# Kernel tuning notes

Measured on AMD Instinct MI355X. Metric: run time of the kernel, lower is better.

## Reference

```python
import jax, jax.numpy as jnp
import numpy as np

EPS = 1e-5

def _gn(x, w, b):
    # GroupNorm with 1 group on [N, C]: normalize each row over C, then affine.
    mu = jnp.mean(x, axis=-1, keepdims=True)
    var = jnp.mean((x - mu) ** 2, axis=-1, keepdims=True)
    return (x - mu) * jax.lax.rsqrt(var + EPS) * w + b

def setup_inputs() -> dict:
    key = jax.random.key(0)
    ks = jax.random.split(key, 24)
    N_AGT, N_CTX, E, D, NC = 50000, 100000, 500000, 128, 2
    s = 0.05  # weight init scale
    inp = {
        "agts": jax.random.normal(ks[0], (N_AGT, D), jnp.float32),
        "ctx": jax.random.normal(ks[1], (N_CTX, D), jnp.float32),
        "agt_ctrs": jax.random.normal(ks[2], (N_AGT, NC), jnp.float32),
        "ctx_ctrs": jax.random.normal(ks[3], (N_CTX, NC), jnp.float32),
        "hi": jax.random.randint(ks[4], (E,), 0, N_AGT, jnp.int32),
        "wi": jax.random.randint(ks[5], (E,), 0, N_CTX, jnp.int32),
        # dist MLP: Linear(2->128, bias) + ReLU, then Linear(128->128 no bias)+GN+ReLU
        "Wd1": jax.random.normal(ks[6], (D, NC), jnp.float32) * s,
        "bd1": jnp.zeros((D,), jnp.float32),
        "Wd2": jax.random.normal(ks[7], (D, D), jnp.float32) * s,
        "gd2w": jnp.ones((D,), jnp.float32), "gd2b": jnp.zeros((D,), jnp.float32),
        # query: Linear(128->128 no bias)+GN+ReLU
        "Wq": jax.random.normal(ks[8], (D, D), jnp.float32) * s,
        "gqw": jnp.ones((D,), jnp.float32), "gqb": jnp.zeros((D,), jnp.float32),
        # ctx MLP: Linear(384->128 no bias)+GN+ReLU, then Linear(128->128 no bias)
        "Wc1": jax.random.normal(ks[9], (D, 3 * D), jnp.float32) * s,
        "gc1w": jnp.ones((D,), jnp.float32), "gc1b": jnp.zeros((D,), jnp.float32),
        "Wc2": jax.random.normal(ks[10], (D, D), jnp.float32) * s,
        # agt linear (no bias), post-scatter GN, final Linear(no bias)+GN
        "Wa": jax.random.normal(ks[11], (D, D), jnp.float32) * s,
        "gnw": jnp.ones((D,), jnp.float32), "gnb": jnp.zeros((D,), jnp.float32),
        "Wl": jax.random.normal(ks[12], (D, D), jnp.float32) * s,
        "glw": jnp.ones((D,), jnp.float32), "glb": jnp.zeros((D,), jnp.float32),
    }
    return inp

def reference(agts, ctx, agt_ctrs, ctx_ctrs, hi, wi,
              Wd1, bd1, Wd2, gd2w, gd2b, Wq, gqw, gqb,
              Wc1, gc1w, gc1b, Wc2, Wa, gnw, gnb, Wl, glw, glb):
    res = agts
    # dist branch: relative center offsets of edges -> MLP
    d = agt_ctrs[hi] - ctx_ctrs[wi]                    # [E, 2]
    d = jax.nn.relu(d @ Wd1.T + bd1)                   # [E, 128]
    d = jax.nn.relu(_gn(d @ Wd2.T, gd2w, gd2b))        # [E, 128]
    # query branch: gathered agent features
    q = jax.nn.relu(_gn(agts[hi] @ Wq.T, gqw, gqb))    # [E, 128]
    # ctx branch: concat(dist, query, gathered ctx) -> MLP
    c = jnp.concatenate([d, q, ctx[wi]], axis=1)       # [E, 384]
    c = jax.nn.relu(_gn(c @ Wc1.T, gc1w, gc1b))        # [E, 128]
    c = c @ Wc2.T                                      # [E, 128]
    # scatter-add messages back to agents
    a = agts @ Wa.T
    a = a.at[hi].add(c)
    a = jax.nn.relu(_gn(a, gnw, gnb))
    a = _gn(a @ Wl.T, glw, glb)
    return jax.nn.relu(a + res)
```

## Files before the change

### kernel.cpp

```cpp
#include <hip/hip_runtime.h>
#include <hip/hip_bf16.h>

#define D 128
#define TM 64
#define APITCH 136
#define WSLICE 16384

typedef __attribute__((ext_vector_type(8))) short short8;
typedef __attribute__((ext_vector_type(4))) float f32x4;
typedef __attribute__((ext_vector_type(2))) float f32x2;

__device__ __forceinline__ short f2bf(float f) {
    union { float f; unsigned u; } v; v.f = f;
    unsigned r = v.u + 0x7fffu + ((v.u >> 16) & 1u);
    return (short)(r >> 16);
}
__device__ __forceinline__ float bflo(unsigned v) {
    union { unsigned u; float f; } t; t.u = v << 16; return t.f;
}
__device__ __forceinline__ float bfhi(unsigned v) {
    union { unsigned u; float f; } t; t.u = v & 0xffff0000u; return t.f;
}
__device__ __forceinline__ unsigned pkbf(float a, float b) {
    return (unsigned)(unsigned short)f2bf(a) | ((unsigned)(unsigned short)f2bf(b) << 16);
}

struct TileLDS {
    short A[TM * APITCH];
    f32x2 red[TM][4][4];
    f32x2 mr[TM];
    int hi_s[TM];
    int wi_s[TM];
};

struct WPA { const float* src[8]; int pitch[8]; int coloff[8]; };

__global__ __launch_bounds__(256)
void k_wprep(WPA a, short* __restrict__ wf) {
    int slice = blockIdx.x & 7, chunk = blockIdx.x >> 3;
    int tid = threadIdx.x, lane = tid & 63;
    int slot = chunk * 4 + (tid >> 6);
    int w = slot >> 3, t = (slot >> 2) & 1, ks = slot & 3;
    int lr = lane & 15, kh = lane >> 4;
    const float* src = a.src[slice];
    int row = w * 32 + t * 16 + lr;
    int col0 = a.coloff[slice] + ks * 32 + kh * 8;
    short8 v;
#pragma unroll
    for (int j = 0; j < 8; ++j) v[j] = f2bf(src[(size_t)row * a.pitch[slice] + col0 + j]);
    *(short8*)&wf[(size_t)slice * WSLICE + ((size_t)slot * 64 + lane) * 8] = v;
}

__device__ __forceinline__ void load_wset_pre(const short* wf, int slice, int w, int lane,
                                              short8 frag[2][4]) {
    const short8* p = (const short8*)(wf + (size_t)slice * WSLICE);
#pragma unroll
    for (int t = 0; t < 2; ++t)
#pragma unroll
        for (int ks = 0; ks < 4; ++ks)
            frag[t][ks] = p[((w * 2 + t) * 4 + ks) * 64 + lane];
}

__device__ __forceinline__ void wave_gemm(const short* A, const short8 frag[2][4],
                                          int lr, int kh, f32x4 acc[4][2]) {
#pragma unroll
    for (int mt = 0; mt < 4; ++mt)
#pragma unroll
        for (int t = 0; t < 2; ++t)
            acc[mt][t] = (f32x4){0.f, 0.f, 0.f, 0.f};
#pragma unroll
    for (int ks = 0; ks < 4; ++ks) {
        short8 a[4];
#pragma unroll
        for (int mt = 0; mt < 4; ++mt)
            a[mt] = *(const short8*)&A[(mt * 16 + lr) * APITCH + ks * 32 + kh * 8];
#pragma unroll
        for (int mt = 0; mt < 4; ++mt)
#pragma unroll
            for (int t = 0; t < 2; ++t)
                acc[mt][t] = __builtin_amdgcn_mfma_f32_16x16x32_bf16(a[mt], frag[t][ks], acc[mt][t], 0, 0, 0);
    }
}

__device__ __forceinline__ void store_acc_global(float* Y, long rbase, int M,
                                                 const f32x4 acc[4][2], int lane, int w) {
    int lr = lane & 15, hh = lane >> 4;
#pragma unroll
    for (int mt = 0; mt < 4; ++mt)
#pragma unroll
        for (int t = 0; t < 2; ++t)
#pragma unroll
            for (int r = 0; r < 4; ++r) {
                int row = mt * 16 + hh * 4 + r;
                if (rbase + row < M)
                    Y[(size_t)(rbase + row) * D + w * 32 + t * 16 + lr] = acc[mt][t][r];
            }
}

__device__ __forceinline__ void store_acc_pk(unsigned* Y, long rbase, int M,
                                             const f32x4 acc[4][2], int lane, int w) {
    int lr = lane & 15, hh = lane >> 4;
#pragma unroll
    for (int mt = 0; mt < 4; ++mt)
#pragma unroll
        for (int r = 0; r < 4; ++r) {
            int row = mt * 16 + hh * 4 + r;
            if (rbase + row < M)
                Y[(size_t)(rbase + row) * 64 + w * 16 + lr] = pkbf(acc[mt][0][r], acc[mt][1][r]);
        }
}

__device__ __forceinline__ void gn_stats(TileLDS& L, const f32x4 acc[4][2],
                                         int tid, int lane, int w) {
    int lr = lane & 15, hh = lane >> 4;
#pragma unroll
    for (int mt = 0; mt < 4; ++mt)
#pragma unroll
        for (int r = 0; r < 4; ++r) {
            float s = acc[mt][0][r] + acc[mt][1][r];
            float q = acc[mt][0][r] * acc[mt][0][r] + acc[mt][1][r] * acc[mt][1][r];
            s += __shfl_xor(s, 1); q += __shfl_xor(q, 1);
            s += __shfl_xor(s, 2); q += __shfl_xor(q, 2);
            if ((lr & 3) == mt) {
                int row = mt * 16 + hh * 4 + r;
                L.red[row][w][lr >> 2] = (f32x2){s, q};
            }
        }
    __syncthreads();
    if (tid < TM) {
        float s = 0.f, q = 0.f;
        const f32x2* p = (const f32x2*)L.red[tid];
#pragma unroll
        for (int i = 0; i < 16; ++i) { f32x2 v = p[i]; s += v[0]; q += v[1]; }
        float mu = s * (1.f / 128.f);
        float var = q * (1.f / 128.f) - mu * mu;
        L.mr[tid] = (f32x2){mu, rsqrtf(var + 1e-5f)};
    }
    __syncthreads();
}

__device__ __forceinline__ void gn_reg(TileLDS& L, const f32x4 acc[4][2],
                                       float gw0, float gb0, float gw1, float gb1,
                                       int tid, int lane, int w) {
    gn_stats(L, acc, tid, lane, w);
    int lr = lane & 15, hh = lane >> 4, n0 = w * 32;
#pragma unroll
    for (int mt = 0; mt < 4; ++mt)
#pragma unroll
        for (int r = 0; r < 4; ++r) {
            int row = mt * 16 + hh * 4 + r;
            f32x2 m = L.mr[row];
            float v0 = (acc[mt][0][r] - m[0]) * m[1] * gw0 + gb0;
            float v1 = (acc[mt][1][r] - m[0]) * m[1] * gw1 + gb1;
            L.A[row * APITCH + n0 + lr]      = f2bf(fmaxf(v0, 0.f));
            L.A[row * APITCH + n0 + 16 + lr] = f2bf(fmaxf(v1, 0.f));
        }
    __syncthreads();
}

__device__ __forceinline__ void stage_rows_to_A(TileLDS& L, const float* X, long rbase, int M, int tid) {
#pragma unroll
    for (int it = 0; it < 8; ++it) {
        int chunk = tid + it * 256;
        int row = chunk >> 5, c4 = chunk & 31;
        long r = rbase + row;
        float4 v = (r < M) ? *(const float4*)&X[(size_t)r * D + c4 * 4] : make_float4(0.f, 0.f, 0.f, 0.f);
        short* a = &L.A[row * APITCH + c4 * 4];
        a[0] = f2bf(v.x); a[1] = f2bf(v.y); a[2] = f2bf(v.z); a[3] = f2bf(v.w);
    }
}

__global__ void k_hist(const int* __restrict__ hi, int* __restrict__ cnt, int E) {
    int i = blockIdx.x * 256 + threadIdx.x;
    if (i < E) atomicAdd(&cnt[hi[i]], 1);
}

__global__ void k_scan(const int* __restrict__ cnt, int* __restrict__ offs,
                       int* __restrict__ cursor, int n) {
    __shared__ int wsum[4];
    __shared__ int carry_s;
    int tid = threadIdx.x, lane = tid & 63, w = tid >> 6;
    if (tid == 0) carry_s = 0;
    __syncthreads();
    for (int base = 0; base < n; base += 256) {
        int i = base + tid;
        int v = (i < n) ? cnt[i] : 0;
        int x = v;
#pragma unroll
        for (int d = 1; d < 64; d <<= 1) {
            int t = __shfl_up(x, d);
            if (lane >= d) x += t;
        }
        if (lane == 63) wsum[w] = x;
        __syncthreads();
        int woff = 0;
        for (int j = 0; j < w; ++j) woff += wsum[j];
        int carry = carry_s;
        int excl = carry + woff + x - v;
        if (i < n) { offs[i] = excl; cursor[i] = excl; }
        __syncthreads();
        if (tid == 255) carry_s = carry + woff + x;
        __syncthreads();
    }
    if (tid == 0) offs[n] = carry_s;
}

__global__ void k_fill(const int* __restrict__ hi, int* __restrict__ cursor,
                       int* __restrict__ eidx, int E) {
    int i = blockIdx.x * 256 + threadIdx.x;
    if (i < E) {
        int p = atomicAdd(&cursor[hi[i]], 1);
        eidx[p] = i;
    }
}

__global__ __launch_bounds__(256, 3)
void k_qpath(const float* __restrict__ agts, const short* __restrict__ wf,
             const float* __restrict__ gqw, const float* __restrict__ gqb,
             unsigned* __restrict__ qp32, float* __restrict__ abuf, int M, int ntiles) {
    __shared__ TileLDS L;
    int tid = threadIdx.x;
    int lane = tid & 63, w = tid >> 6;
    int lr = lane & 15, kh = lane >> 4;
    int n0 = w * 32;
    short8 fa[2][4], fq[2][4], fcq[2][4];
    load_wset_pre(wf, 0, w, lane, fa);
    load_wset_pre(wf, 1, w, lane, fq);
    load_wset_pre(wf, 3, w, lane, fcq);
    float gw0 = gqw[n0 + lr], gw1 = gqw[n0 + 16 + lr];
    float gb0 = gqb[n0 + lr], gb1 = gqb[n0 + 16 + lr];

    for (int tile = blockIdx.x; tile < ntiles; tile += gridDim.x) {
        long rbase = (long)tile * TM;
        stage_rows_to_A(L, agts, rbase, M, tid);
        __syncthreads();
        f32x4 acc[4][2];
        wave_gemm(L.A, fa, lr, kh, acc);
        store_acc_global(abuf, rbase, M, acc, lane, w);
        wave_gemm(L.A, fq, lr, kh, acc);
        gn_reg(L, acc, gw0, gb0, gw1, gb1, tid, lane, w);
        wave_gemm(L.A, fcq, lr, kh, acc);
        store_acc_pk(qp32, rbase, M, acc, lane, w);
        __syncthreads();
    }
}

__global__ __launch_bounds__(256, 4)
void k_ctx(const float* __restrict__ ctx, const short* __restrict__ wf,
           unsigned* __restrict__ cp32, int M, int ntiles) {
    __shared__ TileLDS L;
    int tid = threadIdx.x;
    int lane = tid & 63, w = tid >> 6;
    int lr = lane & 15, kh = lane >> 4;
    short8 fc[2][4];
    load_wset_pre(wf, 4, w, lane, fc);
    for (int tile = blockIdx.x; tile < ntiles; tile += gridDim.x) {
        long rbase = (long)tile * TM;
        stage_rows_to_A(L, ctx, rbase, M, tid);
        __syncthreads();
        f32x4 acc[4][2];
        wave_gemm(L.A, fc, lr, kh, acc);
        store_acc_pk(cp32, rbase, M, acc, lane, w);
        __syncthreads();
    }
}

__global__ __launch_bounds__(256, 3)
void k_edge(const float* __restrict__ agt_ctrs, const float* __restrict__ ctx_ctrs,
            const int* __restrict__ hi, const int* __restrict__ wi,
            const float* __restrict__ Wd1, const float* __restrict__ bd1,
            const short* __restrict__ wf,
            const float* __restrict__ gd2w, const float* __restrict__ gd2b,
            const float* __restrict__ gc1w, const float* __restrict__ gc1b,
            const unsigned* __restrict__ qp32, const unsigned* __restrict__ cp32,
            short* __restrict__ ebuf, int E, int ntiles) {
    __shared__ TileLDS L;
    int tid = threadIdx.x;
    int lane = tid & 63, w = tid >> 6;
    int lr = lane & 15, kh = lane >> 4;
    int n0 = w * 32;
    short8 fd2[2][4], fc1[2][4], fc2[2][4];
    load_wset_pre(wf, 5, w, lane, fd2);
    load_wset_pre(wf, 2, w, lane, fc1);
    load_wset_pre(wf, 6, w, lane, fc2);
    float g2w0 = gd2w[n0 + lr], g2w1 = gd2w[n0 + 16 + lr];
    float g2b0 = gd2b[n0 + lr], g2b1 = gd2b[n0 + 16 + lr];
    float g1w0 = gc1w[n0 + lr], g1w1 = gc1w[n0 + 16 + lr];
    float g1b0 = gc1b[n0 + lr], g1b1 = gc1b[n0 + 16 + lr];

    for (int tile = blockIdx.x; tile < ntiles; tile += gridDim.x) {
        long ebase = (long)tile * TM;
        if (tid < TM) {
            long e = ebase + tid;
            L.hi_s[tid] = (e < E) ? hi[e] : 0;
            L.wi_s[tid] = (e < E) ? wi[e] : 0;
        }
        {
            int row = tid >> 2, q4 = tid & 3;
            long e = ebase + row;
            bool valid = e < E;
            float dd0 = 0.f, dd1 = 0.f;
            if (valid) {
                int h = hi[e], c = wi[e];
                dd0 = agt_ctrs[h * 2 + 0] - ctx_ctrs[c * 2 + 0];
                dd1 = agt_ctrs[h * 2 + 1] - ctx_ctrs[c * 2 + 1];
            }
#pragma unroll
            for (int cb = 0; cb < 4; ++cb) {
                short8 ov;
#pragma unroll
                for (int j = 0; j < 8; ++j) {
                    int c = q4 * 32 + cb * 8 + j;
                    float v = valid ? fmaxf(Wd1[c * 2 + 0] * dd0 + Wd1[c * 2 + 1] * dd1 + bd1[c], 0.f) : 0.f;
                    ov[j] = f2bf(v);
                }
                *(short8*)&L.A[row * APITCH + q4 * 32 + cb * 8] = ov;
            }
        }
        __syncthreads();
        f32x4 acc[4][2];
        wave_gemm(L.A, fd2, lr, kh, acc);
        gn_reg(L, acc, g2w0, g2b0, g2w1, g2b1, tid, lane, w);
        wave_gemm(L.A, fc1, lr, kh, acc);
#pragma unroll
        for (int mt = 0; mt < 4; ++mt)
#pragma unroll
            for (int r = 0; r < 4; ++r) {
                int row = mt * 16 + kh * 4 + r;
                unsigned vq = qp32[(size_t)L.hi_s[row] * 64 + w * 16 + lr];
                unsigned vc = cp32[(size_t)L.wi_s[row] * 64 + w * 16 + lr];
                acc[mt][0][r] += bflo(vq) + bflo(vc);
                acc[mt][1][r] += bfhi(vq) + bfhi(vc);
            }
        gn_reg(L, acc, g1w0, g1b0, g1w1, g1b1, tid, lane, w);
        wave_gemm(L.A, fc2, lr, kh, acc);
#pragma unroll
        for (int mt = 0; mt < 4; ++mt)
#pragma unroll
            for (int r = 0; r < 4; ++r) {
                int erow = mt * 16 + kh * 4 + r;
                long e = ebase + erow;
                if (e < E) {
                    short* dst = ebuf + (size_t)e * D;
                    dst[n0 + lr]      = f2bf(acc[mt][0][r]);
                    dst[n0 + 16 + lr] = f2bf(acc[mt][1][r]);
                }
            }
        __syncthreads();
    }
}

__global__ __launch_bounds__(256, 4)
void k_final(const float* __restrict__ abuf, const float* __restrict__ agts,
             const short* __restrict__ ebuf, const int* __restrict__ offs,
             const int* __restrict__ eidx, const short* __restrict__ wf,
             const float* __restrict__ gnw, const float* __restrict__ gnb,
             const float* __restrict__ glw, const float* __restrict__ glb,
             float* __restrict__ out, int M, int ntiles) {
    __shared__ TileLDS L;
    int tid = threadIdx.x;
    int lane = tid & 63, w = tid >> 6;
    int lr = lane & 15, kh = lane >> 4;
    int n0 = w * 32;
    short8 fl[2][4];
    load_wset_pre(wf, 7, w, lane, fl);
    float gw0 = glw[n0 + lr], gw1 = glw[n0 + 16 + lr];
    float gb0 = glb[n0 + lr], gb1 = glb[n0 + 16 + lr];

    for (int tile = blockIdx.x; tile < ntiles; tile += gridDim.x) {
        long rbase = (long)tile * TM;
        int row = tid >> 2, q4 = tid & 3;
        long r = rbase + row;
        float x[32];
        {
            const float4* src = (const float4*)(abuf + (size_t)r * D + q4 * 32);
#pragma unroll
            for (int i = 0; i < 8; ++i) {
                float4 v = (r < M) ? src[i] : make_float4(0.f, 0.f, 0.f, 0.f);
                x[i * 4 + 0] = v.x; x[i * 4 + 1] = v.y; x[i * 4 + 2] = v.z; x[i * 4 + 3] = v.w;
            }
            if (r < M) {
                int s0 = offs[r], e1 = offs[r + 1];
                for (int p = s0; p < e1; ++p) {
                    int e = eidx[p];
                    const unsigned* er = (const unsigned*)(ebuf + (size_t)e * D + q4 * 32);
#pragma unroll
                    for (int j = 0; j < 16; ++j) {
                        unsigned v = er[j];
                        x[j * 2 + 0] += bflo(v);
                        x[j * 2 + 1] += bfhi(v);
                    }
                }
            }
            float s = 0.f, q = 0.f;
#pragma unroll
            for (int i = 0; i < 32; ++i) { s += x[i]; q += x[i] * x[i]; }
            L.red[row][q4][0] = (f32x2){s, q};
        }
        __syncthreads();
        if (tid < TM) {
            float s = 0.f, q = 0.f;
#pragma unroll
            for (int i = 0; i < 4; ++i) { f32x2 v = L.red[tid][i][0]; s += v[0]; q += v[1]; }
            float mu = s * (1.f / 128.f);
            float var = q * (1.f / 128.f) - mu * mu;
            L.mr[tid] = (f32x2){mu, rsqrtf(var + 1e-5f)};
        }
        __syncthreads();
        {
            f32x2 m = L.mr[row];
#pragma unroll
            for (int cb = 0; cb < 4; ++cb) {
                short8 ov;
#pragma unroll
                for (int j = 0; j < 8; ++j) {
                    int c = q4 * 32 + cb * 8 + j;
                    float v = (x[cb * 8 + j] - m[0]) * m[1] * gnw[c] + gnb[c];
                    ov[j] = f2bf(fmaxf(v, 0.f));
                }
                *(short8*)&L.A[row * APITCH + q4 * 32 + cb * 8] = ov;
            }
        }
        __syncthreads();
        f32x4 acc[4][2];
        wave_gemm(L.A, fl, lr, kh, acc);
        gn_stats(L, acc, tid, lane, w);
#pragma unroll
        for (int mt = 0; mt < 4; ++mt)
#pragma unroll
            for (int rr = 0; rr < 4; ++rr) {
                int orow = mt * 16 + kh * 4 + rr;
                long gr = rbase + orow;
                if (gr < M) {
                    f32x2 m = L.mr[orow];
                    float v0 = (acc[mt][0][rr] - m[0]) * m[1] * gw0 + gb0;
                    float v1 = (acc[mt][1][rr] - m[0]) * m[1] * gw1 + gb1;
                    v0 += agts[(size_t)gr * D + n0 + lr];
                    v1 += agts[(size_t)gr * D + n0 + 16 + lr];
                    out[(size_t)gr * D + n0 + lr]      = fmaxf(v0, 0.f);
                    out[(size_t)gr * D + n0 + 16 + lr] = fmaxf(v1, 0.f);
                }
            }
        __syncthreads();
    }
}

extern "C" void kernel_launch(void* const* d_in, const int* in_sizes, int n_in,
                              void* d_out, int out_size, void* d_ws, size_t ws_size,
                              hipStream_t stream) {
    const float* agts     = (const float*)d_in[0];
    const float* ctx      = (const float*)d_in[1];
    const float* agt_ctrs = (const float*)d_in[2];
    const float* ctx_ctrs = (const float*)d_in[3];
    const int*   hi       = (const int*)d_in[4];
    const int*   wi       = (const int*)d_in[5];
    const float* Wd1 = (const float*)d_in[6];
    const float* bd1 = (const float*)d_in[7];
    const float* Wd2 = (const float*)d_in[8];
    const float* gd2w = (const float*)d_in[9];
    const float* gd2b = (const float*)d_in[10];
    const float* Wq  = (const float*)d_in[11];
    const float* gqw = (const float*)d_in[12];
    const float* gqb = (const float*)d_in[13];
    const float* Wc1 = (const float*)d_in[14];
    const float* gc1w = (const float*)d_in[15];
    const float* gc1b = (const float*)d_in[16];
    const float* Wc2 = (const float*)d_in[17];
    const float* Wa  = (const float*)d_in[18];
    const float* gnw = (const float*)d_in[19];
    const float* gnb = (const float*)d_in[20];
    const float* Wl  = (const float*)d_in[21];
    const float* glw = (const float*)d_in[22];
    const float* glb = (const float*)d_in[23];

    int N_AGT = in_sizes[0] / D;
    int N_CTX = in_sizes[1] / D;
    int E     = in_sizes[4];
    float* out = (float*)d_out;

    short*    wf   = (short*)d_ws;
    unsigned* qp32 = (unsigned*)(wf + 8 * WSLICE);
    unsigned* cp32 = qp32 + (size_t)N_AGT * 64;
    float*    abuf = (float*)(cp32 + (size_t)N_CTX * 64);
    short*    ebuf = (short*)(abuf + (size_t)N_AGT * D);
    int*      cnt    = (int*)(ebuf + (size_t)E * D);
    int*      offs   = cnt + N_AGT;
    int*      cursor = offs + N_AGT + 1;
    int*      eidx   = cursor + N_AGT;

    int tq = (N_AGT + TM - 1) / TM;
    int tc = (N_CTX + TM - 1) / TM;
    int te = (E + TM - 1) / TM;
    int ge = (E + 255) / 256;
    int gq = tq < 768 ? tq : 768;
    int gc = tc < 768 ? tc : 768;
    int gE = te < 1536 ? te : 1536;
    int gf = tq < 768 ? tq : 768;

    WPA wpa;
    wpa.src[0] = Wa;  wpa.pitch[0] = 128; wpa.coloff[0] = 0;
    wpa.src[1] = Wq;  wpa.pitch[1] = 128; wpa.coloff[1] = 0;
    wpa.src[2] = Wc1; wpa.pitch[2] = 384; wpa.coloff[2] = 0;
    wpa.src[3] = Wc1; wpa.pitch[3] = 384; wpa.coloff[3] = 128;
    wpa.src[4] = Wc1; wpa.pitch[4] = 384; wpa.coloff[4] = 256;
    wpa.src[5] = Wd2; wpa.pitch[5] = 128; wpa.coloff[5] = 0;
    wpa.src[6] = Wc2; wpa.pitch[6] = 128; wpa.coloff[6] = 0;
    wpa.src[7] = Wl;  wpa.pitch[7] = 128; wpa.coloff[7] = 0;

    hipMemsetAsync(cnt, 0, (size_t)N_AGT * sizeof(int), stream);
    k_wprep<<<64, 256, 0, stream>>>(wpa, wf);
    k_hist<<<ge, 256, 0, stream>>>(hi, cnt, E);
    k_scan<<<1, 256, 0, stream>>>(cnt, offs, cursor, N_AGT);
    k_fill<<<ge, 256, 0, stream>>>(hi, cursor, eidx, E);

    k_qpath<<<gq, 256, 0, stream>>>(agts, wf, gqw, gqb, qp32, abuf, N_AGT, tq);
    k_ctx<<<gc, 256, 0, stream>>>(ctx, wf, cp32, N_CTX, tc);
    k_edge<<<gE, 256, 0, stream>>>(agt_ctrs, ctx_ctrs, hi, wi, Wd1, bd1, wf,
                                   gd2w, gd2b, gc1w, gc1b, qp32, cp32, ebuf, E, te);
    k_final<<<gf, 256, 0, stream>>>(abuf, agts, ebuf, offs, eidx, wf,
                                    gnw, gnb, glw, glb, out, N_AGT, tq);
}
```

Baseline: 870.0 us.

## Process edges in agent-sorted order and write packed bf16 edge messages

The fill kernel now writes hi and wi permuted into agent-sorted order instead of an edge-index list. k_edge processes edges in that order, so k_final can read each agent's messages as one contiguous stretch of the edge buffer without the eidx indirection, and the q-feature gathers in k_edge get better locality. k_edge also stores each column pair as one packed 32-bit bf16 word instead of two 16-bit stores, and k_final's unpacking is changed to match. The cost is an extra sorted wi array, and an edge order that depends on atomic order, which may change summation order but not the result beyond rounding.

```diff
diff --git a/kernel.cpp b/kernel.cpp
--- a/kernel.cpp
+++ b/kernel.cpp
@@ -205,12 +205,15 @@
     if (tid == 0) offs[n] = carry_s;
 }
 
-__global__ void k_fill(const int* __restrict__ hi, int* __restrict__ cursor,
-                       int* __restrict__ eidx, int E) {
+__global__ void k_fill(const int* __restrict__ hi, const int* __restrict__ wi,
+                       int* __restrict__ cursor,
+                       int* __restrict__ hi_srt, int* __restrict__ wi_srt, int E) {
     int i = blockIdx.x * 256 + threadIdx.x;
     if (i < E) {
-        int p = atomicAdd(&cursor[hi[i]], 1);
-        eidx[p] = i;
+        int h = hi[i];
+        int p = atomicAdd(&cursor[h], 1);
+        hi_srt[p] = h;
+        wi_srt[p] = wi[i];
     }
 }
 
@@ -267,13 +270,13 @@
 
 __global__ __launch_bounds__(256, 3)
 void k_edge(const float* __restrict__ agt_ctrs, const float* __restrict__ ctx_ctrs,
-            const int* __restrict__ hi, const int* __restrict__ wi,
+            const int* __restrict__ hi_srt, const int* __restrict__ wi_srt,
             const float* __restrict__ Wd1, const float* __restrict__ bd1,
             const short* __restrict__ wf,
             const float* __restrict__ gd2w, const float* __restrict__ gd2b,
             const float* __restrict__ gc1w, const float* __restrict__ gc1b,
             const unsigned* __restrict__ qp32, const unsigned* __restrict__ cp32,
-            short* __restrict__ ebuf, int E, int ntiles) {
+            unsigned* __restrict__ ebuf32, int E, int ntiles) {
     __shared__ TileLDS L;
     int tid = threadIdx.x;
     int lane = tid & 63, w = tid >> 6;
@@ -292,8 +295,8 @@
         long ebase = (long)tile * TM;
         if (tid < TM) {
             long e = ebase + tid;
-            L.hi_s[tid] = (e < E) ? hi[e] : 0;
-            L.wi_s[tid] = (e < E) ? wi[e] : 0;
+            L.hi_s[tid] = (e < E) ? hi_srt[e] : 0;
+            L.wi_s[tid] = (e < E) ? wi_srt[e] : 0;
         }
         {
             int row = tid >> 2, q4 = tid & 3;
@@ -301,7 +304,7 @@
             bool valid = e < E;
             float dd0 = 0.f, dd1 = 0.f;
             if (valid) {
-                int h = hi[e], c = wi[e];
+                int h = hi_srt[e], c = wi_srt[e];
                 dd0 = agt_ctrs[h * 2 + 0] - ctx_ctrs[c * 2 + 0];
                 dd1 = agt_ctrs[h * 2 + 1] - ctx_ctrs[c * 2 + 1];
             }
@@ -340,11 +343,8 @@
             for (int r = 0; r < 4; ++r) {
                 int erow = mt * 16 + kh * 4 + r;
                 long e = ebase + erow;
-                if (e < E) {
-                    short* dst = ebuf + (size_t)e * D;
-                    dst[n0 + lr]      = f2bf(acc[mt][0][r]);
-                    dst[n0 + 16 + lr] = f2bf(acc[mt][1][r]);
-                }
+                if (e < E)
+                    ebuf32[(size_t)e * 64 + w * 16 + lr] = pkbf(acc[mt][0][r], acc[mt][1][r]);
             }
         __syncthreads();
     }
@@ -352,8 +352,8 @@
 
 __global__ __launch_bounds__(256, 4)
 void k_final(const float* __restrict__ abuf, const float* __restrict__ agts,
-             const short* __restrict__ ebuf, const int* __restrict__ offs,
-             const int* __restrict__ eidx, const short* __restrict__ wf,
+             const unsigned* __restrict__ ebuf32, const int* __restrict__ offs,
+             const short* __restrict__ wf,
              const float* __restrict__ gnw, const float* __restrict__ gnb,
              const float* __restrict__ glw, const float* __restrict__ glb,
              float* __restrict__ out, int M, int ntiles) {
@@ -382,13 +382,12 @@
             if (r < M) {
                 int s0 = offs[r], e1 = offs[r + 1];
                 for (int p = s0; p < e1; ++p) {
-                    int e = eidx[p];
-                    const unsigned* er = (const unsigned*)(ebuf + (size_t)e * D + q4 * 32);
+                    const unsigned* er = ebuf32 + (size_t)p * 64 + q4 * 16;
 #pragma unroll
                     for (int j = 0; j < 16; ++j) {
                         unsigned v = er[j];
-                        x[j * 2 + 0] += bflo(v);
-                        x[j * 2 + 1] += bfhi(v);
+                        x[j]      += bflo(v);
+                        x[16 + j] += bfhi(v);
                     }
                 }
             }
@@ -478,15 +477,16 @@
     int E     = in_sizes[4];
     float* out = (float*)d_out;
 
-    short*    wf   = (short*)d_ws;
-    unsigned* qp32 = (unsigned*)(wf + 8 * WSLICE);
-    unsigned* cp32 = qp32 + (size_t)N_AGT * 64;
-    float*    abuf = (float*)(cp32 + (size_t)N_CTX * 64);
-    short*    ebuf = (short*)(abuf + (size_t)N_AGT * D);
-    int*      cnt    = (int*)(ebuf + (size_t)E * D);
+    short*    wf     = (short*)d_ws;
+    unsigned* qp32   = (unsigned*)(wf + 8 * WSLICE);
+    unsigned* cp32   = qp32 + (size_t)N_AGT * 64;
+    float*    abuf   = (float*)(cp32 + (size_t)N_CTX * 64);
+    unsigned* ebuf32 = (unsigned*)(abuf + (size_t)N_AGT * D);
+    int*      cnt    = (int*)(ebuf32 + (size_t)E * 64);
     int*      offs   = cnt + N_AGT;
     int*      cursor = offs + N_AGT + 1;
-    int*      eidx   = cursor + N_AGT;
+    int*      hi_srt = cursor + N_AGT;
+    int*      wi_srt = hi_srt + E;
 
     int tq = (N_AGT + TM - 1) / TM;
     int tc = (N_CTX + TM - 1) / TM;
@@ -511,12 +511,12 @@
     k_wprep<<<64, 256, 0, stream>>>(wpa, wf);
     k_hist<<<ge, 256, 0, stream>>>(hi, cnt, E);
     k_scan<<<1, 256, 0, stream>>>(cnt, offs, cursor, N_AGT);
-    k_fill<<<ge, 256, 0, stream>>>(hi, cursor, eidx, E);
+    k_fill<<<ge, 256, 0, stream>>>(hi, wi, cursor, hi_srt, wi_srt, E);
 
     k_qpath<<<gq, 256, 0, stream>>>(agts, wf, gqw, gqb, qp32, abuf, N_AGT, tq);
     k_ctx<<<gc, 256, 0, stream>>>(ctx, wf, cp32, N_CTX, tc);
-    k_edge<<<gE, 256, 0, stream>>>(agt_ctrs, ctx_ctrs, hi, wi, Wd1, bd1, wf,
-                                   gd2w, gd2b, gc1w, gc1b, qp32, cp32, ebuf, E, te);
-    k_final<<<gf, 256, 0, stream>>>(abuf, agts, ebuf, offs, eidx, wf,
+    k_edge<<<gE, 256, 0, stream>>>(agt_ctrs, ctx_ctrs, hi_srt, wi_srt, Wd1, bd1, wf,
+                                   gd2w, gd2b, gc1w, gc1b, qp32, cp32, ebuf32, E, te);
+    k_final<<<gf, 256, 0, stream>>>(abuf, agts, ebuf32, offs, wf,
                                     gnw, gnb, glw, glb, out, N_AGT, tq);
 }
```

Measured after the change: 859.4 us. Within noise of the previous version (-1.2%).
